# Kernel optimization log

Measured on AMD Instinct MI355X. Metric: run time of the kernel, lower is better.

## Reference

```python
import jax, jax.numpy as jnp
import numpy as np

BLK = 46  # hardcoded block size in the original module
EPS = 1e-5


def setup_inputs() -> dict:
    key = jax.random.key(0)
    ks = jax.random.split(key, 13)
    N, C, Ci = 128, 512, 256
    return {
        "ori_feature": jax.random.normal(ks[0], (N, C, BLK), jnp.float32),
        "bn_gamma": jax.random.uniform(ks[1], (C,), jnp.float32),
        "bn_beta": jax.random.normal(ks[2], (C,), jnp.float32),
        "bn_mean": jax.random.normal(ks[3], (C,), jnp.float32),
        "bn_var": jax.random.uniform(ks[4], (C,), jnp.float32),
        "theta_w": jax.random.normal(ks[5], (Ci, C), jnp.float32) * 0.02,
        "theta_b": jax.random.normal(ks[6], (Ci,), jnp.float32) * 0.02,
        "phi_w": jax.random.normal(ks[7], (Ci, C), jnp.float32) * 0.02,
        "phi_b": jax.random.normal(ks[8], (Ci,), jnp.float32) * 0.02,
        "g_w": jax.random.normal(ks[9], (Ci, C), jnp.float32) * 0.02,
        "g_b": jax.random.normal(ks[10], (Ci,), jnp.float32) * 0.02,
        "W_w": jax.random.normal(ks[11], (C, Ci), jnp.float32) * 0.02,
        "W_b": jax.random.normal(ks[12], (C,), jnp.float32) * 0.02,
    }


def reference(ori_feature, bn_gamma, bn_beta, bn_mean, bn_var,
              theta_w, theta_b, phi_w, phi_b, g_w, g_b, W_w, W_b):
    N, C, num = ori_feature.shape  # (N, C, 46)
    # BatchNorm1d (inference-style, per-channel) + ReLU
    inv = bn_gamma / jnp.sqrt(bn_var + EPS)
    feat = jax.nn.relu(ori_feature * inv[None, :, None]
                       + (bn_beta - bn_mean * inv)[None, :, None])
    feat = feat.transpose(0, 2, 1).reshape(N * num, C)  # (T, C)
    x_theta = feat @ theta_w.T + theta_b  # (T, Ci)
    x_phi = feat @ phi_w.T + phi_b        # (T, Ci)
    attn = x_theta @ x_phi.T              # (T, T)
    # block-diagonal masking: entries within the same 46-token block set to -1000
    blk = jnp.arange(N * num) // num
    attn = jnp.where(blk[:, None] == blk[None, :], jnp.float32(-1000.0), attn)
    f_div_C = jax.nn.softmax(attn, axis=-1)
    g_x = feat @ g_w.T + g_b              # (T, Ci)
    y = f_div_C @ g_x                     # (T, Ci)
    W_y = (y @ W_w.T + W_b).reshape(N, num, C)
    att_fea = ori_feature.transpose(0, 2, 1) + W_y  # (N, 46, C)
    return att_fea, f_div_C
```

## Files before the change

### kernel.cpp

```cpp
#include <hip/hip_runtime.h>
#include <math.h>

#define N_BATCH 128
#define C_DIM   512
#define BLKSZ   46
#define T_DIM   (N_BATCH * BLKSZ)
#define CI      256
#define EPS_BN  1e-5f
#define NCB     (T_DIM / 128)

typedef __attribute__((ext_vector_type(8))) short bf16x8;
typedef __attribute__((ext_vector_type(4))) float f32x4;

__device__ __forceinline__ short f2bf(float f) {
    union { float f; unsigned u; } v; v.f = f;
    unsigned r = v.u + 0x7fffu + ((v.u >> 16) & 1u);
    return (short)(r >> 16);
}

__device__ __forceinline__ float h2f(unsigned short h) {
    _Float16 x; __builtin_memcpy(&x, &h, 2); return (float)x;
}
__device__ __forceinline__ unsigned short f2h(float f) {
    _Float16 x = (_Float16)f; unsigned short u; __builtin_memcpy(&u, &x, 2); return u;
}

__device__ __forceinline__ void gload16(const void* g, void* l) {
    __builtin_amdgcn_global_load_lds((__attribute__((address_space(1))) void*)g,
                                     (__attribute__((address_space(3))) void*)l,
                                     16, 0, 0);
}

template <int A> struct avec_sel { using t = float4; };
template <> struct avec_sel<2> { using t = ushort4; };

__global__ __launch_bounds__(256) void bn_relu_kernel(
    const float* __restrict__ ori, const float* __restrict__ gamma,
    const float* __restrict__ beta, const float* __restrict__ mean,
    const float* __restrict__ var, short* __restrict__ feat)
{
    __shared__ short tile[256 * BLKSZ];
    const int n = blockIdx.y;
    const int c0 = blockIdx.x * 256;
    const int tid = threadIdx.x;
    for (int i = tid; i < 256 * BLKSZ; i += 256) {
        int cl = i / BLKSZ, b = i - cl * BLKSZ;
        int c = c0 + cl;
        float inv = gamma[c] * rsqrtf(var[c] + EPS_BN);
        float v = ori[((size_t)n * C_DIM + c) * BLKSZ + b] * inv + (beta[c] - mean[c] * inv);
        tile[cl * BLKSZ + b] = f2bf(fmaxf(v, 0.0f));
    }
    __syncthreads();
    for (int i = tid; i < BLKSZ * 256; i += 256) {
        int b = i >> 8, cl = i & 255;
        feat[(size_t)(n * BLKSZ + b) * C_DIM + c0 + cl] = tile[cl * BLKSZ + b];
    }
}

__global__ __launch_bounds__(256) void cvt_kernel(
    const float* __restrict__ thw, const float* __restrict__ phw,
    const float* __restrict__ gw, const float* __restrict__ Ww,
    const float* __restrict__ thb, const float* __restrict__ phb,
    const float* __restrict__ gb,
    short* __restrict__ wall, short* __restrict__ wW, float* __restrict__ bcat)
{
    const int i = blockIdx.x * 256 + threadIdx.x;
    const float* src[4] = {thw, phw, gw, Ww};
    short* dst[4] = {wall, wall + 256 * 512, wall + 512 * 512, wW};
    #pragma unroll
    for (int m = 0; m < 4; ++m) {
        float4 v = *(const float4*)(src[m] + (size_t)i * 4);
        short4 t = make_short4(f2bf(v.x), f2bf(v.y), f2bf(v.z), f2bf(v.w));
        *(short4*)(dst[m] + (size_t)i * 4) = t;
    }
    if (blockIdx.x == 0) {
        bcat[threadIdx.x] = thb[threadIdx.x];
        bcat[threadIdx.x + 256] = phb[threadIdx.x];
        bcat[threadIdx.x + 512] = gb[threadIdx.x];
    }
}

template <int EPI, int ACVT, int BM, int BN, int OCC = 2>
__global__ __launch_bounds__(256, OCC) void gemm_nt(
    const void* __restrict__ Avoid, const short* __restrict__ B,
    const float* __restrict__ bias, void* __restrict__ Cvoid,
    int M, int Nn, int K, int lda, int ldb, int nsplit,
    const float* __restrict__ ori,
    float* __restrict__ stats, const float* __restrict__ rowstat,
    float* __restrict__ fout)
{
    constexpr int NWC = BN / 64;
    constexpr int NWR = 4 / NWC;
    constexpr int MI  = BM / (NWR * 16);
    constexpr int NBB = (ACVT != 0) ? 3 : 2;
    static_assert((EPI != 5 && EPI != 6 && EPI != 7) || NWC == 2, "stats/split epilogue assumes NWC==2");
    static_assert(ACVT == 0 || (BN == 256 && BM == 32), "pipelined ACVT path geometry");
    static_assert(ACVT != 0 || (BM / 64 + BN / 64 == 4), "vmcnt(4) assumes 4 gloads/stage");
    __shared__ short As[2 * BM * 32];
    __shared__ short Bs[NBB * BN * 32];
    const int tid = threadIdx.x;
    const int w = tid >> 6, lane = tid & 63;

    int bx = blockIdx.x, by = blockIdx.y;
    if constexpr (EPI == 5 || EPI == 6) {
        const int nwg = gridDim.x * gridDim.y;
        const int orig = by * gridDim.x + bx;
        const int q = nwg >> 3, r = nwg & 7;
        const int xcd = orig & 7, idx = orig >> 3;
        const int wg = (xcd < r ? xcd * (q + 1) : r * (q + 1) + (xcd - r) * q) + idx;
        bx = wg % gridDim.x; by = wg / gridDim.x;
    }
    const int m0 = by * BM, n0 = bx * BN;
    const int wr = w / NWC, wc = w % NWC;
    const int wrow = wr * (MI * 16);

    const int kper = K / 32 / nsplit;
    const int kt0 = blockIdx.z * kper, kt1 = kt0 + kper;
    const int ktn = kt1 - kt0;

    f32x4 acc[MI][4] = {};

    const int sr = tid >> 2;
    const int sc = (tid & 3) * 8;
    const short* Ab = (const short*)Avoid;

    if constexpr (ACVT == 0) {
        auto stageAB = [&](int kt, int buf) {
            const int k0 = kt * 32;
            #pragma unroll
            for (int p = 0; p < BM / 64; ++p)
                gload16(Ab + (size_t)(m0 + p * 64 + sr) * lda + k0 + sc,
                        &As[buf * BM * 32 + (p * 64 + sr) * 32 + sc]);
            #pragma unroll
            for (int p = 0; p < BN / 64; ++p)
                gload16(B + (size_t)(n0 + p * 64 + sr) * ldb + k0 + sc,
                        &Bs[buf * BN * 32 + (p * 64 + sr) * 32 + sc]);
        };
        stageAB(kt0, 0);
        if (ktn > 1) stageAB(kt0 + 1, 1);
        if (ktn > 1) asm volatile("s_waitcnt vmcnt(4)\n\ts_barrier" ::: "memory");
        else         asm volatile("s_waitcnt vmcnt(0)\n\ts_barrier" ::: "memory");

        for (int t = 0; t < ktn; ++t) {
            const int cur = t & 1;
            bf16x8 af[MI], bfr[4];
            #pragma unroll
            for (int i = 0; i < MI; ++i)
                af[i] = *(bf16x8*)&As[cur * BM * 32 + (wrow + i * 16 + (lane & 15)) * 32 + (lane >> 4) * 8];
            #pragma unroll
            for (int j = 0; j < 4; ++j)
                bfr[j] = *(bf16x8*)&Bs[cur * BN * 32 + (wc * 64 + j * 16 + (lane & 15)) * 32 + (lane >> 4) * 8];
            asm volatile("s_waitcnt lgkmcnt(0)\n\ts_barrier" ::: "memory");
            if (t + 2 < ktn) stageAB(kt0 + t + 2, cur);
            #pragma unroll
            for (int i = 0; i < MI; ++i)
                #pragma unroll
                for (int j = 0; j < 4; ++j)
                    acc[i][j] = __builtin_amdgcn_mfma_f32_16x16x32_bf16(af[i], bfr[j], acc[i][j], 0, 0, 0);
            if (t + 2 < ktn)      asm volatile("s_waitcnt vmcnt(4)\n\ts_barrier" ::: "memory");
            else if (t + 1 < ktn) asm volatile("s_waitcnt vmcnt(0)\n\ts_barrier" ::: "memory");
        }
    } else {
        constexpr int EPT = BM * 32 / 256;
        static_assert(EPT == 4, "pipelined ACVT path assumes EPT==4");
        constexpr int TPR = 32 / EPT;
        const int a_r = tid / TPR;
        const int a_c = (tid % TPR) * EPT;
        float2 st = ((const float2*)rowstat)[m0 + a_r];
        const float rm = st.x, rz = st.y;
        using AV = typename avec_sel<ACVT>::t;
        const AV* Arow = (const AV*)((const char*)Avoid
                         + ((size_t)(m0 + a_r) * lda) * (ACVT == 2 ? 2 : 4));
        float* frow = fout + (size_t)(m0 + a_r) * lda;

        auto stageB = [&](int kt, int buf) {
            #pragma unroll
            for (int p = 0; p < BN / 64; ++p)
                gload16(B + (size_t)(n0 + p * 64 + sr) * ldb + kt * 32 + sc,
                        &Bs[buf * BN * 32 + (p * 64 + sr) * 32 + sc]);
        };

        AV hva = Arow[(kt0 * 32 + a_c) / 4];
        AV hvb = hva;
        stageB(kt0, 0);
        if (ktn > 1) { hvb = Arow[((kt0 + 1) * 32 + a_c) / 4]; stageB(kt0 + 1, 1); }
        if (ktn > 1) asm volatile("s_waitcnt vmcnt(4)" ::: "memory");
        else         asm volatile("s_waitcnt vmcnt(0)" ::: "memory");

        int curB = 0, stB = 2;
        for (int t = 0; t < ktn; ++t) {
            const int kt = kt0 + t;
            const int curA = t & 1;
            AV v = hva; hva = hvb;
            float4 vf;
            if constexpr (ACVT == 2) {
                vf.x = h2f(v.x); vf.y = h2f(v.y); vf.z = h2f(v.z); vf.w = h2f(v.w);
            } else {
                vf.x = v.x; vf.y = v.y; vf.z = v.z; vf.w = v.w;
            }
            float4 e;
            e.x = expf(vf.x - rm) * rz; e.y = expf(vf.y - rm) * rz;
            e.z = expf(vf.z - rm) * rz; e.w = expf(vf.w - rm) * rz;
            *(float4*)(frow + kt * 32 + a_c) = e;
            short4 tq = make_short4(f2bf(e.x), f2bf(e.y), f2bf(e.z), f2bf(e.w));
            *(short4*)&As[curA * BM * 32 + a_r * 32 + a_c] = tq;
            if (t + 2 < ktn) hvb = Arow[((kt + 2) * 32 + a_c) / 4];

            asm volatile("s_waitcnt lgkmcnt(0)\n\ts_barrier" ::: "memory");
            if (t + 2 < ktn) stageB(kt + 2, stB);

            bf16x8 af[MI], bfr[4];
            #pragma unroll
            for (int i = 0; i < MI; ++i)
                af[i] = *(bf16x8*)&As[curA * BM * 32 + (wrow + i * 16 + (lane & 15)) * 32 + (lane >> 4) * 8];
            #pragma unroll
            for (int j = 0; j < 4; ++j)
                bfr[j] = *(bf16x8*)&Bs[curB * BN * 32 + (wc * 64 + j * 16 + (lane & 15)) * 32 + (lane >> 4) * 8];
            #pragma unroll
            for (int i = 0; i < MI; ++i)
                #pragma unroll
                for (int j = 0; j < 4; ++j)
                    acc[i][j] = __builtin_amdgcn_mfma_f32_16x16x32_bf16(af[i], bfr[j], acc[i][j], 0, 0, 0);

            if (t + 2 < ktn)      asm volatile("s_waitcnt vmcnt(6)\n\ts_barrier" ::: "memory");
            else if (t + 1 < ktn) asm volatile("s_waitcnt vmcnt(1)\n\ts_barrier" ::: "memory");
            else                  asm volatile("s_waitcnt vmcnt(0)\n\ts_barrier" ::: "memory");
            curB = (curB == 2) ? 0 : curB + 1;
            stB  = (stB == 2) ? 0 : stB + 1;
        }
    }

    const int col = lane & 15, rowq = lane >> 4;

    if constexpr (EPI == 5 || EPI == 6) {
        __shared__ float sm[NWC][BM];
        __shared__ float ss[NWC][BM];
        int cbj[4];
        #pragma unroll
        for (int j = 0; j < 4; ++j)
            cbj[j] = (n0 + wc * 64 + j * 16 + col) / BLKSZ;
        #pragma unroll
        for (int i = 0; i < MI; ++i) {
            #pragma unroll
            for (int r = 0; r < 4; ++r) {
                const int trow = wrow + i * 16 + rowq * 4 + r;
                const int grow = m0 + trow;
                const int rb = grow / BLKSZ;
                float vj[4];
                float vmax = -1e30f;
                #pragma unroll
                for (int j = 0; j < 4; ++j) {
                    float v = acc[i][j][r];
                    if (cbj[j] == rb) v = -30000.0f;
                    const size_t idx = (size_t)grow * Nn + (n0 + wc * 64 + j * 16 + col);
                    if constexpr (EPI == 6) {
                        unsigned short hh = f2h(v);
                        ((unsigned short*)Cvoid)[idx] = hh;
                        v = h2f(hh);
                    } else {
                        ((float*)Cvoid)[idx] = v;
                    }
                    vj[j] = v;
                    vmax = fmaxf(vmax, v);
                }
                #pragma unroll
                for (int off = 1; off < 16; off <<= 1)
                    vmax = fmaxf(vmax, __shfl_xor(vmax, off));
                float s = 0.f;
                #pragma unroll
                for (int j = 0; j < 4; ++j) s += expf(vj[j] - vmax);
                #pragma unroll
                for (int off = 1; off < 16; off <<= 1)
                    s += __shfl_xor(s, off);
                if (col == 0) { sm[wc][trow] = vmax; ss[wc][trow] = s; }
            }
        }
        __syncthreads();
        if (tid < BM) {
            const float ma = sm[0][tid], mb = sm[1][tid];
            const float mx = fmaxf(ma, mb);
            const float S = ss[0][tid] * expf(ma - mx) + ss[1][tid] * expf(mb - mx);
            ((float2*)stats)[(size_t)bx * M + (m0 + tid)] = make_float2(mx, S);
        }
    } else if constexpr (EPI == 7) {
        if (n0 < 512) {
            #pragma unroll
            for (int i = 0; i < MI; ++i)
                #pragma unroll
                for (int j = 0; j < 4; ++j)
                    #pragma unroll
                    for (int r = 0; r < 4; ++r) {
                        const int grow = m0 + wrow + i * 16 + rowq * 4 + r;
                        const int gcol = n0 + wc * 64 + j * 16 + col;
                        ((short*)Cvoid)[(size_t)grow * 512 + gcol] =
                            f2bf(acc[i][j][r] + bias[gcol]);
                    }
        } else {
            short* gxTp = (short*)stats;
            #pragma unroll
            for (int i = 0; i < MI; ++i)
                #pragma unroll
                for (int j = 0; j < 4; ++j) {
                    const int grow0 = m0 + wrow + i * 16 + rowq * 4;
                    const int gcol = n0 + wc * 64 + j * 16 + col;
                    const float bv = bias[gcol];
                    short4 t = make_short4(
                        f2bf(acc[i][j][0] + bv), f2bf(acc[i][j][1] + bv),
                        f2bf(acc[i][j][2] + bv), f2bf(acc[i][j][3] + bv));
                    *(short4*)&gxTp[(size_t)(gcol - 512) * T_DIM + grow0] = t;
                }
        }
    } else {
        #pragma unroll
        for (int i = 0; i < MI; ++i) {
            #pragma unroll
            for (int j = 0; j < 4; ++j) {
                #pragma unroll
                for (int r = 0; r < 4; ++r) {
                    const int grow = m0 + wrow + i * 16 + rowq * 4 + r;
                    const int gcol = n0 + wc * 64 + j * 16 + col;
                    const float v = acc[i][j][r];
                    if (EPI == 1) {
                        ((short*)Cvoid)[(size_t)grow * Nn + gcol] = f2bf(v + bias[gcol]);
                    } else if (EPI == 2) {
                        ((short*)Cvoid)[(size_t)grow * Nn + gcol] = f2bf(v + bias[grow]);
                    } else if (EPI == 3) {
                        ((unsigned short*)Cvoid)[(size_t)blockIdx.z * M * Nn + (size_t)grow * Nn + gcol] = f2h(v);
                    } else {
                        const int nb = grow / BLKSZ, bb = grow - nb * BLKSZ;
                        ((float*)Cvoid)[(size_t)grow * Nn + gcol] =
                            v + bias[gcol] + ori[((size_t)nb * C_DIM + gcol) * BLKSZ + bb];
                    }
                }
            }
        }
    }
}

__global__ __launch_bounds__(256) void combine_stats_kernel(
    const float* __restrict__ stats, float* __restrict__ rowstat)
{
    const int row = blockIdx.x * 256 + threadIdx.x;
    float m = -1e30f, Z = 0.f;
    for (int cb = 0; cb < NCB; ++cb) {
        float2 p = ((const float2*)stats)[(size_t)cb * T_DIM + row];
        float nm = fmaxf(m, p.x);
        Z = Z * expf(m - nm) + p.y * expf(p.x - nm);
        m = nm;
    }
    ((float2*)rowstat)[row] = make_float2(m, 1.0f / Z);
}

__global__ __launch_bounds__(256) void reduce_y_kernel(
    const unsigned short* __restrict__ part, short* __restrict__ y, int ns)
{
    const size_t i = (size_t)blockIdx.x * 256 + threadIdx.x;
    float s0 = 0.f, s1 = 0.f, s2 = 0.f, s3 = 0.f;
    for (int z = 0; z < ns; ++z) {
        ushort4 v = *(const ushort4*)(part + (size_t)z * T_DIM * CI + i * 4);
        s0 += h2f(v.x); s1 += h2f(v.y); s2 += h2f(v.z); s3 += h2f(v.w);
    }
    short4 t = make_short4(f2bf(s0), f2bf(s1), f2bf(s2), f2bf(s3));
    *(short4*)(y + i * 4) = t;
}

extern "C" void kernel_launch(void* const* d_in, const int* in_sizes, int n_in,
                              void* d_out, int out_size, void* d_ws, size_t ws_size,
                              hipStream_t stream)
{
    const float* ori     = (const float*)d_in[0];
    const float* gamma   = (const float*)d_in[1];
    const float* beta    = (const float*)d_in[2];
    const float* mean    = (const float*)d_in[3];
    const float* var     = (const float*)d_in[4];
    const float* theta_w = (const float*)d_in[5];
    const float* theta_b = (const float*)d_in[6];
    const float* phi_w   = (const float*)d_in[7];
    const float* phi_b   = (const float*)d_in[8];
    const float* g_w     = (const float*)d_in[9];
    const float* g_b     = (const float*)d_in[10];
    const float* W_w     = (const float*)d_in[11];
    const float* W_b     = (const float*)d_in[12];

    float* out = (float*)d_out;
    float* P   = out + (size_t)T_DIM * C_DIM;

    char* wsb = (char*)d_ws;
    short* feat = (short*)wsb;  wsb += (size_t)T_DIM * C_DIM * 2;
    short* xcat = (short*)wsb;  wsb += (size_t)T_DIM * 512 * 2;
    short* gxT  = (short*)wsb;  wsb += (size_t)CI * T_DIM * 2;
    short* wall = (short*)wsb;  wsb += (size_t)768 * C_DIM * 2;
    short* wW   = (short*)wsb;  wsb += (size_t)C_DIM * CI * 2;
    float* bcat = (float*)wsb;  wsb += 768 * 4;
    short* ybf  = (short*)wsb;  wsb += (size_t)T_DIM * CI * 2;
    float* rowstat = (float*)wsb; wsb += (size_t)T_DIM * 8;

    const size_t base   = (size_t)(wsb - (char*)d_ws);
    const size_t p16sz  = (size_t)T_DIM * T_DIM * 2;
    const size_t ypsz4  = 4u * (size_t)T_DIM * CI * 2u;
    const bool bigws = ws_size >= base + p16sz + ypsz4;

    bn_relu_kernel<<<dim3(2, 128), 256, 0, stream>>>(ori, gamma, beta, mean, var, feat);
    cvt_kernel<<<128, 256, 0, stream>>>(theta_w, phi_w, g_w, W_w, theta_b, phi_b, g_b,
                                        wall, wW, bcat);

    gemm_nt<7, 0, 128, 128><<<dim3(6, T_DIM / 128), 256, 0, stream>>>(
        feat, wall, bcat, xcat, T_DIM, 768, C_DIM, C_DIM, C_DIM, 1, nullptr,
        (float*)gxT, nullptr, nullptr);

    if (bigws) {
        unsigned short* p16 = (unsigned short*)wsb;
        unsigned short* ypart = (unsigned short*)(wsb + p16sz);
        float* stats = (float*)ypart;

        gemm_nt<6, 0, 128, 128><<<dim3(T_DIM / 128, T_DIM / 128), 256, 0, stream>>>(
            xcat, xcat + CI, nullptr, p16, T_DIM, T_DIM, CI, 512, 512, 1, nullptr,
            stats, nullptr, nullptr);
        combine_stats_kernel<<<T_DIM / 256, 256, 0, stream>>>(stats, rowstat);
        gemm_nt<3, 2, 32, 256, 3><<<dim3(1, T_DIM / 32, 4), 256, 0, stream>>>(
            p16, gxT, nullptr, ypart, T_DIM, CI, T_DIM, T_DIM, T_DIM, 4, nullptr,
            nullptr, rowstat, P);
        reduce_y_kernel<<<(T_DIM * CI / 4) / 256, 256, 0, stream>>>(ypart, ybf, 4);
    } else {
        unsigned short* ypart = (unsigned short*)wsb;
        float* stats = (float*)wsb;
        const int ns = (ws_size >= base + ypsz4) ? 4 : 2;

        gemm_nt<5, 0, 128, 128><<<dim3(T_DIM / 128, T_DIM / 128), 256, 0, stream>>>(
            xcat, xcat + CI, nullptr, P, T_DIM, T_DIM, CI, 512, 512, 1, nullptr,
            stats, nullptr, nullptr);
        combine_stats_kernel<<<T_DIM / 256, 256, 0, stream>>>(stats, rowstat);
        gemm_nt<3, 1, 32, 256, 3><<<dim3(1, T_DIM / 32, ns), 256, 0, stream>>>(
            P, gxT, nullptr, ypart, T_DIM, CI, T_DIM, T_DIM, T_DIM, ns, nullptr,
            nullptr, rowstat, P);
        reduce_y_kernel<<<(T_DIM * CI / 4) / 256, 256, 0, stream>>>(ypart, ybf, ns);
    }

    gemm_nt<4, 0, 128, 128><<<dim3(C_DIM / 128, T_DIM / 128), 256, 0, stream>>>(
        ybf, wW, W_b, out, T_DIM, C_DIM, CI, CI, CI, 1, ori,
        nullptr, nullptr, nullptr);
}
```

Baseline: 331.2 us.

## Fuse prep kernels, inline softmax stat combine, retile projection GEMMs, add setprio

Merges the BN/ReLU transpose and weight-conversion kernels into one launch, and folds the row-stat combine into the P·g GEMM prologue so that kernel launch goes away. The projection and output GEMMs switch to 64x128 tiles with occupancy 3, and the wait helper now generalizes the vmcnt to the number of loads per stage. MFMA loops are bracketed with s_setprio to favour compute waves. The trade-off is that every P·g block now recomputes its rows' stats redundantly from the partial stats, and the smaller tiles lower data reuse per block.

Result: no change. 330.8 us (-0.1%).

```diff
diff --git a/kernel.cpp b/kernel.cpp
--- a/kernel.cpp
+++ b/kernel.cpp
@@ -31,52 +31,62 @@
                                      16, 0, 0);
 }
 
+template <int V> __device__ __forceinline__ void wait_vm_bar() {
+    if constexpr (V == 0) asm volatile("s_waitcnt vmcnt(0)\n\ts_barrier" ::: "memory");
+    else if constexpr (V == 1) asm volatile("s_waitcnt vmcnt(1)\n\ts_barrier" ::: "memory");
+    else if constexpr (V == 2) asm volatile("s_waitcnt vmcnt(2)\n\ts_barrier" ::: "memory");
+    else if constexpr (V == 3) asm volatile("s_waitcnt vmcnt(3)\n\ts_barrier" ::: "memory");
+    else if constexpr (V == 4) asm volatile("s_waitcnt vmcnt(4)\n\ts_barrier" ::: "memory");
+    else if constexpr (V == 6) asm volatile("s_waitcnt vmcnt(6)\n\ts_barrier" ::: "memory");
+    else asm volatile("s_waitcnt vmcnt(8)\n\ts_barrier" ::: "memory");
+}
+
 template <int A> struct avec_sel { using t = float4; };
 template <> struct avec_sel<2> { using t = ushort4; };
 
-__global__ __launch_bounds__(256) void bn_relu_kernel(
+__global__ __launch_bounds__(256) void prep_kernel(
     const float* __restrict__ ori, const float* __restrict__ gamma,
     const float* __restrict__ beta, const float* __restrict__ mean,
-    const float* __restrict__ var, short* __restrict__ feat)
-{
-    __shared__ short tile[256 * BLKSZ];
-    const int n = blockIdx.y;
-    const int c0 = blockIdx.x * 256;
-    const int tid = threadIdx.x;
-    for (int i = tid; i < 256 * BLKSZ; i += 256) {
-        int cl = i / BLKSZ, b = i - cl * BLKSZ;
-        int c = c0 + cl;
-        float inv = gamma[c] * rsqrtf(var[c] + EPS_BN);
-        float v = ori[((size_t)n * C_DIM + c) * BLKSZ + b] * inv + (beta[c] - mean[c] * inv);
-        tile[cl * BLKSZ + b] = f2bf(fmaxf(v, 0.0f));
-    }
-    __syncthreads();
-    for (int i = tid; i < BLKSZ * 256; i += 256) {
-        int b = i >> 8, cl = i & 255;
-        feat[(size_t)(n * BLKSZ + b) * C_DIM + c0 + cl] = tile[cl * BLKSZ + b];
-    }
-}
-
-__global__ __launch_bounds__(256) void cvt_kernel(
+    const float* __restrict__ var, short* __restrict__ feat,
     const float* __restrict__ thw, const float* __restrict__ phw,
     const float* __restrict__ gw, const float* __restrict__ Ww,
     const float* __restrict__ thb, const float* __restrict__ phb,
     const float* __restrict__ gb,
     short* __restrict__ wall, short* __restrict__ wW, float* __restrict__ bcat)
 {
-    const int i = blockIdx.x * 256 + threadIdx.x;
-    const float* src[4] = {thw, phw, gw, Ww};
-    short* dst[4] = {wall, wall + 256 * 512, wall + 512 * 512, wW};
-    #pragma unroll
-    for (int m = 0; m < 4; ++m) {
-        float4 v = *(const float4*)(src[m] + (size_t)i * 4);
-        short4 t = make_short4(f2bf(v.x), f2bf(v.y), f2bf(v.z), f2bf(v.w));
-        *(short4*)(dst[m] + (size_t)i * 4) = t;
-    }
-    if (blockIdx.x == 0) {
-        bcat[threadIdx.x] = thb[threadIdx.x];
-        bcat[threadIdx.x + 256] = phb[threadIdx.x];
-        bcat[threadIdx.x + 512] = gb[threadIdx.x];
+    __shared__ short tile[256 * BLKSZ];
+    const int tid = threadIdx.x;
+    if (blockIdx.x < 256) {
+        const int n = blockIdx.x >> 1;
+        const int c0 = (blockIdx.x & 1) * 256;
+        for (int i = tid; i < 256 * BLKSZ; i += 256) {
+            int cl = i / BLKSZ, b = i - cl * BLKSZ;
+            int c = c0 + cl;
+            float inv = gamma[c] * rsqrtf(var[c] + EPS_BN);
+            float v = ori[((size_t)n * C_DIM + c) * BLKSZ + b] * inv + (beta[c] - mean[c] * inv);
+            tile[cl * BLKSZ + b] = f2bf(fmaxf(v, 0.0f));
+        }
+        __syncthreads();
+        for (int i = tid; i < BLKSZ * 256; i += 256) {
+            int b = i >> 8, cl = i & 255;
+            feat[(size_t)(n * BLKSZ + b) * C_DIM + c0 + cl] = tile[cl * BLKSZ + b];
+        }
+    } else {
+        const int bx2 = blockIdx.x - 256;
+        const int i = bx2 * 256 + tid;
+        const float* src[4] = {thw, phw, gw, Ww};
+        short* dst[4] = {wall, wall + 256 * 512, wall + 512 * 512, wW};
+        #pragma unroll
+        for (int m = 0; m < 4; ++m) {
+            float4 v = *(const float4*)(src[m] + (size_t)i * 4);
+            short4 t = make_short4(f2bf(v.x), f2bf(v.y), f2bf(v.z), f2bf(v.w));
+            *(short4*)(dst[m] + (size_t)i * 4) = t;
+        }
+        if (bx2 == 0) {
+            bcat[tid] = thb[tid];
+            bcat[tid + 256] = phb[tid];
+            bcat[tid + 512] = gb[tid];
+        }
     }
 }
 
@@ -93,9 +103,9 @@
     constexpr int NWR = 4 / NWC;
     constexpr int MI  = BM / (NWR * 16);
     constexpr int NBB = (ACVT != 0) ? 3 : 2;
+    constexpr int GL  = BM / 64 + BN / 64;
     static_assert((EPI != 5 && EPI != 6 && EPI != 7) || NWC == 2, "stats/split epilogue assumes NWC==2");
     static_assert(ACVT == 0 || (BN == 256 && BM == 32), "pipelined ACVT path geometry");
-    static_assert(ACVT != 0 || (BM / 64 + BN / 64 == 4), "vmcnt(4) assumes 4 gloads/stage");
     __shared__ short As[2 * BM * 32];
     __shared__ short Bs[NBB * BN * 32];
     const int tid = threadIdx.x;
@@ -138,8 +148,8 @@
         };
         stageAB(kt0, 0);
         if (ktn > 1) stageAB(kt0 + 1, 1);
-        if (ktn > 1) asm volatile("s_waitcnt vmcnt(4)\n\ts_barrier" ::: "memory");
-        else         asm volatile("s_waitcnt vmcnt(0)\n\ts_barrier" ::: "memory");
+        if (ktn > 1) wait_vm_bar<GL>();
+        else         wait_vm_bar<0>();
 
         for (int t = 0; t < ktn; ++t) {
             const int cur = t & 1;
@@ -152,13 +162,15 @@
                 bfr[j] = *(bf16x8*)&Bs[cur * BN * 32 + (wc * 64 + j * 16 + (lane & 15)) * 32 + (lane >> 4) * 8];
             asm volatile("s_waitcnt lgkmcnt(0)\n\ts_barrier" ::: "memory");
             if (t + 2 < ktn) stageAB(kt0 + t + 2, cur);
+            __builtin_amdgcn_s_setprio(1);
             #pragma unroll
             for (int i = 0; i < MI; ++i)
                 #pragma unroll
                 for (int j = 0; j < 4; ++j)
                     acc[i][j] = __builtin_amdgcn_mfma_f32_16x16x32_bf16(af[i], bfr[j], acc[i][j], 0, 0, 0);
-            if (t + 2 < ktn)      asm volatile("s_waitcnt vmcnt(4)\n\ts_barrier" ::: "memory");
-            else if (t + 1 < ktn) asm volatile("s_waitcnt vmcnt(0)\n\ts_barrier" ::: "memory");
+            __builtin_amdgcn_s_setprio(0);
+            if (t + 2 < ktn)      wait_vm_bar<GL>();
+            else if (t + 1 < ktn) wait_vm_bar<0>();
         }
     } else {
         constexpr int EPT = BM * 32 / 256;
@@ -166,8 +178,37 @@
         constexpr int TPR = 32 / EPT;
         const int a_r = tid / TPR;
         const int a_c = (tid % TPR) * EPT;
-        float2 st = ((const float2*)rowstat)[m0 + a_r];
-        const float rm = st.x, rz = st.y;
+
+        float rm, rz;
+        {
+            float2* scr = (float2*)As;
+            const int rr = tid >> 3, cc = tid & 7;
+            float mm = -1e30f, ZZ = 0.f;
+            for (int cb = cc; cb < NCB; cb += 8) {
+                float2 p = ((const float2*)stats)[(size_t)cb * M + (m0 + rr)];
+                float nm = fmaxf(mm, p.x);
+                ZZ = ZZ * expf(mm - nm) + p.y * expf(p.x - nm);
+                mm = nm;
+            }
+            scr[rr * 8 + cc] = make_float2(mm, ZZ);
+            __syncthreads();
+            if (tid < BM) {
+                float m2 = -1e30f, Z2 = 0.f;
+                #pragma unroll
+                for (int c = 0; c < 8; ++c) {
+                    float2 p = scr[tid * 8 + c];
+                    float nm = fmaxf(m2, p.x);
+                    Z2 = Z2 * expf(m2 - nm) + p.y * expf(p.x - nm);
+                    m2 = nm;
+                }
+                scr[256 + tid] = make_float2(m2, 1.0f / Z2);
+            }
+            __syncthreads();
+            float2 st = scr[256 + a_r];
+            rm = st.x; rz = st.y;
+            __syncthreads();
+        }
+
         using AV = typename avec_sel<ACVT>::t;
         const AV* Arow = (const AV*)((const char*)Avoid
                          + ((size_t)(m0 + a_r) * lda) * (ACVT == 2 ? 2 : 4));
@@ -216,11 +257,13 @@
             #pragma unroll
             for (int j = 0; j < 4; ++j)
                 bfr[j] = *(bf16x8*)&Bs[curB * BN * 32 + (wc * 64 + j * 16 + (lane & 15)) * 32 + (lane >> 4) * 8];
+            __builtin_amdgcn_s_setprio(1);
             #pragma unroll
             for (int i = 0; i < MI; ++i)
                 #pragma unroll
                 for (int j = 0; j < 4; ++j)
                     acc[i][j] = __builtin_amdgcn_mfma_f32_16x16x32_bf16(af[i], bfr[j], acc[i][j], 0, 0, 0);
+            __builtin_amdgcn_s_setprio(0);
 
             if (t + 2 < ktn)      asm volatile("s_waitcnt vmcnt(6)\n\ts_barrier" ::: "memory");
             else if (t + 1 < ktn) asm volatile("s_waitcnt vmcnt(1)\n\ts_barrier" ::: "memory");
@@ -337,20 +380,6 @@
     }
 }
 
-__global__ __launch_bounds__(256) void combine_stats_kernel(
-    const float* __restrict__ stats, float* __restrict__ rowstat)
-{
-    const int row = blockIdx.x * 256 + threadIdx.x;
-    float m = -1e30f, Z = 0.f;
-    for (int cb = 0; cb < NCB; ++cb) {
-        float2 p = ((const float2*)stats)[(size_t)cb * T_DIM + row];
-        float nm = fmaxf(m, p.x);
-        Z = Z * expf(m - nm) + p.y * expf(p.x - nm);
-        m = nm;
-    }
-    ((float2*)rowstat)[row] = make_float2(m, 1.0f / Z);
-}
-
 __global__ __launch_bounds__(256) void reduce_y_kernel(
     const unsigned short* __restrict__ part, short* __restrict__ y, int ns)
 {
@@ -393,50 +422,46 @@
     short* wW   = (short*)wsb;  wsb += (size_t)C_DIM * CI * 2;
     float* bcat = (float*)wsb;  wsb += 768 * 4;
     short* ybf  = (short*)wsb;  wsb += (size_t)T_DIM * CI * 2;
-    float* rowstat = (float*)wsb; wsb += (size_t)T_DIM * 8;
+    float* stats = (float*)wsb; wsb += (size_t)NCB * T_DIM * 8;
 
     const size_t base   = (size_t)(wsb - (char*)d_ws);
     const size_t p16sz  = (size_t)T_DIM * T_DIM * 2;
     const size_t ypsz4  = 4u * (size_t)T_DIM * CI * 2u;
     const bool bigws = ws_size >= base + p16sz + ypsz4;
 
-    bn_relu_kernel<<<dim3(2, 128), 256, 0, stream>>>(ori, gamma, beta, mean, var, feat);
-    cvt_kernel<<<128, 256, 0, stream>>>(theta_w, phi_w, g_w, W_w, theta_b, phi_b, g_b,
-                                        wall, wW, bcat);
-
-    gemm_nt<7, 0, 128, 128><<<dim3(6, T_DIM / 128), 256, 0, stream>>>(
+    prep_kernel<<<384, 256, 0, stream>>>(ori, gamma, beta, mean, var, feat,
+                                         theta_w, phi_w, g_w, W_w,
+                                         theta_b, phi_b, g_b, wall, wW, bcat);
+
+    gemm_nt<7, 0, 64, 128, 3><<<dim3(6, T_DIM / 64), 256, 0, stream>>>(
         feat, wall, bcat, xcat, T_DIM, 768, C_DIM, C_DIM, C_DIM, 1, nullptr,
         (float*)gxT, nullptr, nullptr);
 
     if (bigws) {
         unsigned short* p16 = (unsigned short*)wsb;
         unsigned short* ypart = (unsigned short*)(wsb + p16sz);
-        float* stats = (float*)ypart;
-
-        gemm_nt<6, 0, 128, 128><<<dim3(T_DIM / 128, T_DIM / 128), 256, 0, stream>>>(
+
+        gemm_nt<6, 0, 128, 128, 2><<<dim3(T_DIM / 128, T_DIM / 128), 256, 0, stream>>>(
             xcat, xcat + CI, nullptr, p16, T_DIM, T_DIM, CI, 512, 512, 1, nullptr,
             stats, nullptr, nullptr);
-        combine_stats_kernel<<<T_DIM / 256, 256, 0, stream>>>(stats, rowstat);
         gemm_nt<3, 2, 32, 256, 3><<<dim3(1, T_DIM / 32, 4), 256, 0, stream>>>(
             p16, gxT, nullptr, ypart, T_DIM, CI, T_DIM, T_DIM, T_DIM, 4, nullptr,
-            nullptr, rowstat, P);
+            stats, nullptr, P);
         reduce_y_kernel<<<(T_DIM * CI / 4) / 256, 256, 0, stream>>>(ypart, ybf, 4);
     } else {
         unsigned short* ypart = (unsigned short*)wsb;
-        float* stats = (float*)wsb;
         const int ns = (ws_size >= base + ypsz4) ? 4 : 2;
 
-        gemm_nt<5, 0, 128, 128><<<dim3(T_DIM / 128, T_DIM / 128), 256, 0, stream>>>(
+        gemm_nt<5, 0, 128, 128, 2><<<dim3(T_DIM / 128, T_DIM / 128), 256, 0, stream>>>(
             xcat, xcat + CI, nullptr, P, T_DIM, T_DIM, CI, 512, 512, 1, nullptr,
             stats, nullptr, nullptr);
-        combine_stats_kernel<<<T_DIM / 256, 256, 0, stream>>>(stats, rowstat);
         gemm_nt<3, 1, 32, 256, 3><<<dim3(1, T_DIM / 32, ns), 256, 0, stream>>>(
             P, gxT, nullptr, ypart, T_DIM, CI, T_DIM, T_DIM, T_DIM, ns, nullptr,
-            nullptr, rowstat, P);
+            stats, nullptr, P);
         reduce_y_kernel<<<(T_DIM * CI / 4) / 256, 256, 0, stream>>>(ypart, ybf, ns);
     }
 
-    gemm_nt<4, 0, 128, 128><<<dim3(C_DIM / 128, T_DIM / 128), 256, 0, stream>>>(
+    gemm_nt<4, 0, 64, 128, 3><<<dim3(C_DIM / 128, T_DIM / 64), 256, 0, stream>>>(
         ybf, wW, W_b, out, T_DIM, C_DIM, CI, CI, CI, 1, ori,
         nullptr, nullptr, nullptr);
 }
```
